# Performance work log

Hardware: AMD Instinct MI355X
Metric: run time of the kernel (lower is better)

Reference implementation:

```python
import jax, jax.numpy as jnp
import numpy as np

N = 100000      # number of nodes
D = 64          # node_dim
H = 128         # hidden
E = 1600000     # number of undirected edges (each yields 2 directed messages)


def setup_inputs() -> dict:
    key = jax.random.key(0)
    k_nodes, k_edges, k_w1, k_w2 = jax.random.split(key, 4)
    nodes = jax.random.normal(k_nodes, (N, D), dtype=jnp.float32)
    edges = jax.random.randint(k_edges, (E, 2), 0, N, dtype=jnp.int32)
    # msg = Linear(2D, H) -> ReLU -> Linear(H, D); Kaiming-ish init
    W1 = jax.random.normal(k_w1, (2 * D, H), dtype=jnp.float32) * (1.0 / np.sqrt(2 * D))
    b1 = jnp.zeros((H,), dtype=jnp.float32)
    W2 = jax.random.normal(k_w2, (H, D), dtype=jnp.float32) * (1.0 / np.sqrt(H))
    b2 = jnp.zeros((D,), dtype=jnp.float32)
    return {"nodes": nodes, "edges": edges, "W1": W1, "b1": b1, "W2": W2, "b2": b2}


def reference(nodes, edges, W1, b1, W2, b2):
    # nodes: [N, D]; edges: [E, 2] int32
    i = edges[:, 0]
    j = edges[:, 1]
    h_i = nodes[i]            # [E, D] gather
    h_j = nodes[j]            # [E, D] gather

    def mlp(x):               # [E, 2D] -> [E, D]
        return jax.nn.relu(x @ W1 + b1) @ W2 + b2

    m_ij = mlp(jnp.concatenate([h_i, h_j], axis=-1))  # message to node i
    m_ji = mlp(jnp.concatenate([h_j, h_i], axis=-1))  # message to node j

    # out = nodes.clone(); out[i] += m_ij; out[j] += m_ji  (all from ORIGINAL nodes)
    out = nodes \
        + jax.ops.segment_sum(m_ij, i, num_segments=N) \
        + jax.ops.segment_sum(m_ji, j, num_segments=N)
    return out
```

## Files before the change

### kernel.cpp

```cpp
#include <hip/hip_runtime.h>

#define NEDGES 1600000
#define NNODES 100000
#define OVCAP  (1 << 19)

typedef __bf16 bf16x8 __attribute__((ext_vector_type(8)));
typedef __bf16 bf16x4 __attribute__((ext_vector_type(4)));
typedef float f32x4 __attribute__((ext_vector_type(4)));
typedef unsigned short u16x8 __attribute__((ext_vector_type(8)));

__device__ __forceinline__ __bf16 f2bf(float f) {
  unsigned u = __builtin_bit_cast(unsigned, f);
  u += 0x7FFFu + ((u >> 16) & 1u);
  unsigned short s = (unsigned short)(u >> 16);
  return __builtin_bit_cast(__bf16, s);
}


__device__ __forceinline__ void cvt_row(const float* __restrict__ nodes, int t,
                                        __bf16* __restrict__ nbf) {
  float4 v0 = ((const float4*)nodes)[t * 2];
  float4 v1 = ((const float4*)nodes)[t * 2 + 1];
  bf16x8 o;
  o[0] = f2bf(v0.x); o[1] = f2bf(v0.y); o[2] = f2bf(v0.z); o[3] = f2bf(v0.w);
  o[4] = f2bf(v1.x); o[5] = f2bf(v1.y); o[6] = f2bf(v1.z); o[7] = f2bf(v1.w);
  ((bf16x8*)nbf)[t] = o;
}

__device__ __forceinline__ void weight_img(const float* __restrict__ W1,
                                           const float* __restrict__ W2,
                                           int t, __bf16* __restrict__ wimg) {
  if (t < 16384) {
    int k = t >> 7, n = t & 127;
    wimg[n * 128 + (((k >> 3) ^ (n & 15)) << 3) + (k & 7)] = f2bf(W1[t]);
  } else if (t < 24576) {
    int u = t - 16384;
    int k = u >> 6, n = u & 63;
    wimg[16384 + n * 128 + (((k >> 3) ^ (n & 15)) << 3) + (k & 7)] = f2bf(W2[u]);
  }
}


__global__ void zero_k(unsigned* __restrict__ cnt, unsigned* __restrict__ ovn) {
  int g = blockIdx.x * 256 + threadIdx.x;
  if (g < NNODES) cnt[g] = 0u;
  if (g == 0) *ovn = 0u;
}

__global__ void build_k(const float* __restrict__ nodes,
                        const int* __restrict__ edges,
                        const float* __restrict__ W1,
                        const float* __restrict__ W2,
                        unsigned* __restrict__ cnt,
                        unsigned* __restrict__ rec,
                        unsigned* __restrict__ ovf,
                        unsigned* __restrict__ ovn,
                        __bf16* __restrict__ wimg,
                        __bf16* __restrict__ nbf,
                        int cap) {
  const int t = blockIdx.x * 256 + threadIdx.x;
  cvt_row(nodes, t, nbf);
  weight_img(W1, W2, t, wimg);
  int4 e = ((const int4*)edges)[t];
  unsigned s0 = atomicAdd(&cnt[e.x], 1u);
  unsigned s1 = atomicAdd(&cnt[e.y], 1u);
  unsigned s2 = atomicAdd(&cnt[e.z], 1u);
  unsigned s3 = atomicAdd(&cnt[e.w], 1u);
  if ((int)s0 < cap) rec[(long)e.x * cap + s0] = (unsigned)e.y;
  else { unsigned p = atomicAdd(ovn, 1u);
         if (p < OVCAP) { ovf[2 * p] = (unsigned)e.x; ovf[2 * p + 1] = (unsigned)e.y; } }
  if ((int)s1 < cap) rec[(long)e.y * cap + s1] = (unsigned)e.x;
  else { unsigned p = atomicAdd(ovn, 1u);
         if (p < OVCAP) { ovf[2 * p] = (unsigned)e.y; ovf[2 * p + 1] = (unsigned)e.x; } }
  if ((int)s2 < cap) rec[(long)e.z * cap + s2] = (unsigned)e.w;
  else { unsigned p = atomicAdd(ovn, 1u);
         if (p < OVCAP) { ovf[2 * p] = (unsigned)e.z; ovf[2 * p + 1] = (unsigned)e.w; } }
  if ((int)s3 < cap) rec[(long)e.w * cap + s3] = (unsigned)e.z;
  else { unsigned p = atomicAdd(ovn, 1u);
         if (p < OVCAP) { ovf[2 * p] = (unsigned)e.w; ovf[2 * p + 1] = (unsigned)e.z; } }
}

__global__ void ovf_k(const float* __restrict__ nodes,
                      const float* __restrict__ W1, const float* __restrict__ b1,
                      const float* __restrict__ W2, const float* __restrict__ b2,
                      const unsigned* __restrict__ ovf,
                      const unsigned* __restrict__ ovn,
                      float* __restrict__ out) {
  unsigned n = *ovn; if (n > OVCAP) n = OVCAP;
  const unsigned total = n * 64u;
  for (unsigned idx = blockIdx.x * blockDim.x + threadIdx.x; idx < total;
       idx += gridDim.x * blockDim.x) {
    const unsigned r = idx >> 6; const int d = (int)(idx & 63u);
    const int v = (int)ovf[2 * r], u = (int)ovf[2 * r + 1];
    const float* hv = nodes + (long)v * 64;
    const float* hu = nodes + (long)u * 64;
    float md = b2[d];
    for (int h = 0; h < 128; ++h) {
      float s = b1[h];
      for (int k = 0; k < 64; ++k)
        s += hv[k] * W1[k * 128 + h] + hu[k] * W1[(64 + k) * 128 + h];
      s = s > 0.f ? s : 0.f;
      md += s * W2[h * 64 + d];
    }
    atomicAdd(out + (long)v * 64 + d, md);
  }
}

__launch_bounds__(256, 2)
__global__ void gnn_k(const __bf16* __restrict__ nbf,
                      const float* __restrict__ nodes,
                      const unsigned* __restrict__ cntoff,
                      const unsigned* __restrict__ rec,
                      const __bf16* __restrict__ wimg,
                      const float* __restrict__ b1,
                      const float* __restrict__ b2,
                      float* __restrict__ out) {
  __shared__ __align__(16) __bf16 w1t[128 * 128];
  __shared__ __align__(16) __bf16 w2t[64 * 128];
  __shared__ __align__(16) __bf16 hid[4][16 * 128];

  const int tid = threadIdx.x;

  {
    const u16x8* s1 = (const u16x8*)wimg;
    u16x8* d1 = (u16x8*)w1t;
#pragma unroll
    for (int it = 0; it < 8; ++it) d1[it * 256 + tid] = s1[it * 256 + tid];
    const u16x8* s2 = (const u16x8*)(wimg + 16384);
    u16x8* d2 = (u16x8*)w2t;
#pragma unroll
    for (int it = 0; it < 4; ++it) d2[it * 256 + tid] = s2[it * 256 + tid];
  }
  __syncthreads();

  const int lane = tid & 63, wave = tid >> 6;
  const int col = lane & 15, quad = lane >> 4;
  __bf16* myhid = hid[wave];

  const float b2l = b2[lane];

  const int bid = blockIdx.x;
  const int wg = (bid & 7) * 3125 + (bid >> 3);
  const int v = wg * 4 + wave;

  const unsigned c = cntoff[v];
  const int deg = (c < 64u) ? (int)c : 64;
  const long base = (long)v * 64;
  const int ntile = (deg + 15) >> 4;

  int ridx = v;
  if (lane < deg) ridx = (int)rec[base + lane];

  f32x4 accv[8];
  {
    const bf16x8* vrow = (const bf16x8*)(nbf + (long)v * 64);
    const bf16x8 v0f = vrow[quad];
    const bf16x8 v1f = vrow[4 + quad];
#pragma unroll
    for (int nt = 0; nt < 8; ++nt)
      accv[nt] = *(const f32x4*)&b1[nt * 16 + quad * 4];
#pragma unroll
    for (int kt = 0; kt < 2; ++kt) {
      const int kblk = kt * 4 + quad;
      const bf16x8 bx = kt ? v1f : v0f;
#pragma unroll
      for (int nt = 0; nt < 8; ++nt) {
        const int n = nt * 16 + col;
        const bf16x8 aw = *(const bf16x8*)&w1t[n * 128 + ((kblk ^ (n & 15)) << 3)];
        accv[nt] = __builtin_amdgcn_mfma_f32_16x16x32_bf16(aw, bx, accv[nt], 0, 0, 0);
      }
    }
  }

  float part[4] = {0.f, 0.f, 0.f, 0.f};

  bf16x8 a2, a3;
  {
    const int o0n = __shfl(ridx, col, 64);
    const bf16x8* orow = (const bf16x8*)(nbf + (long)o0n * 64);
    a2 = orow[quad]; a3 = orow[4 + quad];
  }

  for (int t = 0; t < ntile; ++t) {
    const int tb = t * 16;

    const int onx = __shfl(ridx, (tb + 16 + col) & 63, 64);
    const bf16x8* prow = (const bf16x8*)(nbf + (long)onx * 64);
    const bf16x8 p2 = prow[quad];
    const bf16x8 p3 = prow[4 + quad];

#pragma unroll
    for (int nt = 0; nt < 8; ++nt) {
      const int n = nt * 16 + col;
      const bf16x8 A2 = *(const bf16x8*)&w1t[n * 128 + (((8 + quad) ^ (n & 15)) << 3)];
      const bf16x8 A3 = *(const bf16x8*)&w1t[n * 128 + (((12 + quad) ^ (n & 15)) << 3)];
      f32x4 h = __builtin_amdgcn_mfma_f32_16x16x32_bf16(A2, a2, accv[nt], 0, 0, 0);
      h = __builtin_amdgcn_mfma_f32_16x16x32_bf16(A3, a3, h, 0, 0, 0);
      bf16x4 hp;
#pragma unroll
      for (int r = 0; r < 4; ++r) {
        float x = h[r];
        hp[r] = f2bf(x > 0.0f ? x : 0.0f);
      }
      const int hblk = nt * 2 + (quad >> 1);
      *(bf16x4*)&myhid[col * 128 + ((hblk ^ col) << 3) + ((quad & 1) << 2)] = hp;
    }

    f32x4 acc2[4];
#pragma unroll
    for (int nt = 0; nt < 4; ++nt) acc2[nt] = (f32x4)0.0f;
#pragma unroll
    for (int kt = 0; kt < 4; ++kt) {
      const int kblk = kt * 4 + quad;
      const bf16x8 ah = *(const bf16x8*)&myhid[col * 128 + ((kblk ^ col) << 3)];
#pragma unroll
      for (int nt = 0; nt < 4; ++nt) {
        const int n = nt * 16 + col;
        const bf16x8 bw = *(const bf16x8*)&w2t[n * 128 + ((kblk ^ (n & 15)) << 3)];
        acc2[nt] = __builtin_amdgcn_mfma_f32_16x16x32_bf16(ah, bw, acc2[nt], 0, 0, 0);
      }
    }

    if (tb + 16 <= deg) {
#pragma unroll
      for (int nt = 0; nt < 4; ++nt)
        part[nt] += (acc2[nt][0] + acc2[nt][1]) + (acc2[nt][2] + acc2[nt][3]);
    } else {
#pragma unroll
      for (int r = 0; r < 4; ++r) {
        const bool valid = (tb + quad * 4 + r) < deg;
#pragma unroll
        for (int nt = 0; nt < 4; ++nt) part[nt] += valid ? acc2[nt][r] : 0.0f;
      }
    }

    a2 = p2; a3 = p3;
  }

#pragma unroll
  for (int nt = 0; nt < 4; ++nt) {
    part[nt] += __shfl_xor(part[nt], 16, 64);
    part[nt] += __shfl_xor(part[nt], 32, 64);
  }
  const float v01 = (quad & 1) ? part[1] : part[0];
  const float v23 = (quad & 1) ? part[3] : part[2];
  const float val = (quad & 2) ? v23 : v01;

  const long o = (long)v * 64 + lane;
  out[o] = nodes[o] + val + (float)deg * b2l;
}

__launch_bounds__(256, 2)
__global__ void gnn_csr_k(const __bf16* __restrict__ nbf,
                          const float* __restrict__ nodes,
                          const unsigned* __restrict__ off,
                          const unsigned* __restrict__ rec,
                          const __bf16* __restrict__ wimg,
                          const float* __restrict__ b1,
                          const float* __restrict__ b2,
                          float* __restrict__ out) {
  __shared__ __align__(16) __bf16 w1t[128 * 128];
  __shared__ __align__(16) __bf16 w2t[64 * 128];
  __shared__ __align__(16) __bf16 hid[4][16 * 128];

  const int tid = threadIdx.x;
  {
    const u16x8* s1 = (const u16x8*)wimg;
    u16x8* d1 = (u16x8*)w1t;
#pragma unroll
    for (int it = 0; it < 8; ++it) d1[it * 256 + tid] = s1[it * 256 + tid];
    const u16x8* s2 = (const u16x8*)(wimg + 16384);
    u16x8* d2 = (u16x8*)w2t;
#pragma unroll
    for (int it = 0; it < 4; ++it) d2[it * 256 + tid] = s2[it * 256 + tid];
  }
  __syncthreads();

  const int lane = tid & 63, wave = tid >> 6;
  const int col = lane & 15, quad = lane >> 4;
  __bf16* myhid = hid[wave];
  const float b2l = b2[lane];

  const int bid = blockIdx.x;
  const int wg = (bid & 7) * 3125 + (bid >> 3);
  const int v = wg * 4 + wave;

  const unsigned o0 = off[v];
  const int deg = (int)(off[v + 1] - o0);
  const long base = (long)o0;
  const int ntile = (deg + 15) >> 4;

  f32x4 accv[8];
  {
    const bf16x8* vrow = (const bf16x8*)(nbf + (long)v * 64);
    const bf16x8 v0f = vrow[quad];
    const bf16x8 v1f = vrow[4 + quad];
#pragma unroll
    for (int nt = 0; nt < 8; ++nt)
      accv[nt] = *(const f32x4*)&b1[nt * 16 + quad * 4];
#pragma unroll
    for (int kt = 0; kt < 2; ++kt) {
      const int kblk = kt * 4 + quad;
      const bf16x8 bx = kt ? v1f : v0f;
#pragma unroll
      for (int nt = 0; nt < 8; ++nt) {
        const int n = nt * 16 + col;
        const bf16x8 aw = *(const bf16x8*)&w1t[n * 128 + ((kblk ^ (n & 15)) << 3)];
        accv[nt] = __builtin_amdgcn_mfma_f32_16x16x32_bf16(aw, bx, accv[nt], 0, 0, 0);
      }
    }
  }

  float part[4] = {0.f, 0.f, 0.f, 0.f};

  bf16x8 a2, a3;
  {
    int o0n = v;
    if (col < deg) o0n = (int)rec[base + col];
    const bf16x8* orow = (const bf16x8*)(nbf + (long)o0n * 64);
    a2 = orow[quad]; a3 = orow[4 + quad];
  }

  for (int t = 0; t < ntile; ++t) {
    const int tb = t * 16;
    int onx = v;
    {
      const int rr = tb + 16 + col;
      if (rr < deg) onx = (int)rec[base + rr];
    }
    const bf16x8* prow = (const bf16x8*)(nbf + (long)onx * 64);
    const bf16x8 p2 = prow[quad];
    const bf16x8 p3 = prow[4 + quad];

#pragma unroll
    for (int nt = 0; nt < 8; ++nt) {
      const int n = nt * 16 + col;
      const bf16x8 A2 = *(const bf16x8*)&w1t[n * 128 + (((8 + quad) ^ (n & 15)) << 3)];
      const bf16x8 A3 = *(const bf16x8*)&w1t[n * 128 + (((12 + quad) ^ (n & 15)) << 3)];
      f32x4 h = __builtin_amdgcn_mfma_f32_16x16x32_bf16(A2, a2, accv[nt], 0, 0, 0);
      h = __builtin_amdgcn_mfma_f32_16x16x32_bf16(A3, a3, h, 0, 0, 0);
      bf16x4 hp;
#pragma unroll
      for (int r = 0; r < 4; ++r) {
        float x = h[r];
        hp[r] = f2bf(x > 0.0f ? x : 0.0f);
      }
      const int hblk = nt * 2 + (quad >> 1);
      *(bf16x4*)&myhid[col * 128 + ((hblk ^ col) << 3) + ((quad & 1) << 2)] = hp;
    }

    f32x4 acc2[4];
#pragma unroll
    for (int nt = 0; nt < 4; ++nt) acc2[nt] = (f32x4)0.0f;
#pragma unroll
    for (int kt = 0; kt < 4; ++kt) {
      const int kblk = kt * 4 + quad;
      const bf16x8 ah = *(const bf16x8*)&myhid[col * 128 + ((kblk ^ col) << 3)];
#pragma unroll
      for (int nt = 0; nt < 4; ++nt) {
        const int n = nt * 16 + col;
        const bf16x8 bw = *(const bf16x8*)&w2t[n * 128 + ((kblk ^ (n & 15)) << 3)];
        acc2[nt] = __builtin_amdgcn_mfma_f32_16x16x32_bf16(ah, bw, acc2[nt], 0, 0, 0);
      }
    }

    if (tb + 16 <= deg) {
#pragma unroll
      for (int nt = 0; nt < 4; ++nt)
        part[nt] += (acc2[nt][0] + acc2[nt][1]) + (acc2[nt][2] + acc2[nt][3]);
    } else {
#pragma unroll
      for (int r = 0; r < 4; ++r) {
        const bool valid = (tb + quad * 4 + r) < deg;
#pragma unroll
        for (int nt = 0; nt < 4; ++nt) part[nt] += valid ? acc2[nt][r] : 0.0f;
      }
    }

    a2 = p2; a3 = p3;
  }

#pragma unroll
  for (int nt = 0; nt < 4; ++nt) {
    part[nt] += __shfl_xor(part[nt], 16, 64);
    part[nt] += __shfl_xor(part[nt], 32, 64);
  }
  const float v01 = (quad & 1) ? part[1] : part[0];
  const float v23 = (quad & 1) ? part[3] : part[2];
  const float val = (quad & 2) ? v23 : v01;

  const long o = (long)v * 64 + lane;
  out[o] = nodes[o] + val + (float)deg * b2l;
}


__global__ void prep_k(const float* __restrict__ nodes,
                       const float* __restrict__ W1,
                       const float* __restrict__ W2,
                       unsigned* __restrict__ cnt,
                       __bf16* __restrict__ wimg,
                       __bf16* __restrict__ nbf) {
  const int t = blockIdx.x * 256 + threadIdx.x;
  cvt_row(nodes, t, nbf);
  if (t < NNODES) cnt[t] = 0u;
  weight_img(W1, W2, t, wimg);
}

__global__ void hist_k(const int* __restrict__ edges, unsigned* __restrict__ cnt) {
  const int t = blockIdx.x * 256 + threadIdx.x;
  int4 e = ((const int4*)edges)[t];
  atomicAdd(&cnt[e.x], 1u); atomicAdd(&cnt[e.y], 1u);
  atomicAdd(&cnt[e.z], 1u); atomicAdd(&cnt[e.w], 1u);
}

__global__ void scanA_k(const unsigned* __restrict__ cnt, unsigned* __restrict__ bsum) {
  __shared__ unsigned s[1024];
  const int tid = threadIdx.x;
  const int g = blockIdx.x * 1024 + tid;
  s[tid] = (g < NNODES) ? cnt[g] : 0u;
  __syncthreads();
  for (int d = 512; d > 0; d >>= 1) {
    if (tid < d) s[tid] += s[tid + d];
    __syncthreads();
  }
  if (tid == 0) bsum[blockIdx.x] = s[0];
}

__global__ void scanB_k(const unsigned* __restrict__ cnt,
                        const unsigned* __restrict__ bsum,
                        unsigned* __restrict__ off, unsigned* __restrict__ cur) {
  __shared__ unsigned s[1024];
  const int tid = threadIdx.x;
  const int b = blockIdx.x;
  const int g = b * 1024 + tid;
  unsigned pfx = 0;
  for (int j = 0; j < b; ++j) pfx += bsum[j];
  const unsigned x = (g < NNODES) ? cnt[g] : 0u;
  s[tid] = x;
  __syncthreads();
  for (int d = 1; d < 1024; d <<= 1) {
    unsigned tv = (tid >= d) ? s[tid - d] : 0u;
    __syncthreads();
    s[tid] += tv;
    __syncthreads();
  }
  const unsigned excl = pfx + s[tid] - x;
  if (g < NNODES) { off[g] = excl; cur[g] = excl; }
  if (g == NNODES - 1) off[NNODES] = excl + x;
}

__global__ void scat_k(const int* __restrict__ edges,
                       unsigned* __restrict__ cur, unsigned* __restrict__ rec) {
  const int t = blockIdx.x * 256 + threadIdx.x;
  int4 e = ((const int4*)edges)[t];
#pragma unroll
  for (int h = 0; h < 2; ++h) {
    const int a = h ? e.z : e.x;
    const int b = h ? e.w : e.y;
    rec[atomicAdd(&cur[a], 1u)] = (unsigned)b;
    rec[atomicAdd(&cur[b], 1u)] = (unsigned)a;
  }
}


__global__ void init_out(const float* __restrict__ nodes, float* __restrict__ out) {
  int i = blockIdx.x * blockDim.x + threadIdx.x;
  ((float4*)out)[i] = ((const float4*)nodes)[i];
}

__launch_bounds__(256, 2)
__global__ void edge_mlp(const float* __restrict__ nodes,
                         const int* __restrict__ edges,
                         const float* __restrict__ W1,
                         const float* __restrict__ b1,
                         const float* __restrict__ W2,
                         const float* __restrict__ b2,
                         float* __restrict__ out) {
  __shared__ __bf16 w1t[128 * 128];
  __shared__ __bf16 w2t[64 * 128];
  __shared__ __bf16 hid[4][16 * 128];

  const int tid = threadIdx.x;

  for (int it = 0; it < 16; ++it) {
    int q = it * 256 + tid;
    int k = q >> 5;
    int nc = (q & 31) << 2;
    float4 v = ((const float4*)W1)[q];
    float vv[4] = {v.x, v.y, v.z, v.w};
#pragma unroll
    for (int c = 0; c < 4; ++c) {
      int n = nc + c;
      int blk = (k >> 3) ^ (n & 15);
      w1t[n * 128 + blk * 8 + (k & 7)] = f2bf(vv[c]);
    }
  }
  for (int it = 0; it < 8; ++it) {
    int q = it * 256 + tid;
    int k = q >> 4;
    int nc = (q & 15) << 2;
    float4 v = ((const float4*)W2)[q];
    float vv[4] = {v.x, v.y, v.z, v.w};
#pragma unroll
    for (int c = 0; c < 4; ++c) {
      int n = nc + c;
      int blk = (k >> 3) ^ (n & 15);
      w2t[n * 128 + blk * 8 + (k & 7)] = f2bf(vv[c]);
    }
  }
  __syncthreads();

  const int lane = tid & 63;
  const int wave = tid >> 6;
  const int col = lane & 15;
  const int quad = lane >> 4;
  __bf16* myhid = hid[wave];

  float b1v[8], b2v[4];
#pragma unroll
  for (int nt = 0; nt < 8; ++nt) b1v[nt] = b1[nt * 16 + col];
#pragma unroll
  for (int nt = 0; nt < 4; ++nt) b2v[nt] = b2[nt * 16 + col];

  for (int t = 0; t < 8; ++t) {
    const int e0 = blockIdx.x * 512 + wave * 128 + t * 16;
    const int e = e0 + col;
    const int ie = edges[2 * e];
    const int je = edges[2 * e + 1];

    bf16x8 af[4];
#pragma unroll
    for (int kt = 0; kt < 4; ++kt) {
      int k = kt * 32 + quad * 8;
      const float* src = (k < 64) ? (nodes + (long)ie * 64 + k)
                                  : (nodes + (long)je * 64 + (k - 64));
      float4 v0 = ((const float4*)src)[0];
      float4 v1 = ((const float4*)src)[1];
      bf16x8 a;
      a[0] = f2bf(v0.x); a[1] = f2bf(v0.y); a[2] = f2bf(v0.z); a[3] = f2bf(v0.w);
      a[4] = f2bf(v1.x); a[5] = f2bf(v1.y); a[6] = f2bf(v1.z); a[7] = f2bf(v1.w);
      af[kt] = a;
    }

#pragma unroll
    for (int dir = 0; dir < 2; ++dir) {
      f32x4 acc[8];
#pragma unroll
      for (int nt = 0; nt < 8; ++nt) acc[nt] = (f32x4)0.0f;
#pragma unroll
      for (int kt = 0; kt < 4; ++kt) {
        int kblk = kt * 4 + quad;
        if (dir) kblk ^= 8;
#pragma unroll
        for (int nt = 0; nt < 8; ++nt) {
          int n = nt * 16 + col;
          const bf16x8 bf = *(const bf16x8*)&w1t[n * 128 + ((kblk ^ (n & 15)) << 3)];
          acc[nt] = __builtin_amdgcn_mfma_f32_16x16x32_bf16(af[kt], bf, acc[nt], 0, 0, 0);
        }
      }
#pragma unroll
      for (int nt = 0; nt < 8; ++nt) {
        int unit = nt * 16 + col;
#pragma unroll
        for (int r = 0; r < 4; ++r) {
          int m = quad * 4 + r;
          float h = acc[nt][r] + b1v[nt];
          h = h > 0.0f ? h : 0.0f;
          myhid[m * 128 + (((unit >> 3) ^ m) << 3) + (unit & 7)] = f2bf(h);
        }
      }

      f32x4 acc2[4];
#pragma unroll
      for (int nt = 0; nt < 4; ++nt) acc2[nt] = (f32x4)0.0f;
#pragma unroll
      for (int kt = 0; kt < 4; ++kt) {
        int kblk = kt * 4 + quad;
        const bf16x8 ah = *(const bf16x8*)&myhid[col * 128 + ((kblk ^ col) << 3)];
#pragma unroll
        for (int nt = 0; nt < 4; ++nt) {
          int n = nt * 16 + col;
          const bf16x8 bf = *(const bf16x8*)&w2t[n * 128 + ((kblk ^ (n & 15)) << 3)];
          acc2[nt] = __builtin_amdgcn_mfma_f32_16x16x32_bf16(ah, bf, acc2[nt], 0, 0, 0);
        }
      }

#pragma unroll
      for (int r = 0; r < 4; ++r) {
        int em = quad * 4 + r;
        int node = __shfl(dir == 0 ? ie : je, em, 64);
        float* dst = out + (long)node * 64;
#pragma unroll
        for (int nt = 0; nt < 4; ++nt) {
          atomicAdd(dst + nt * 16 + col, acc2[nt][r] + b2v[nt]);
        }
      }
    }
  }
}


extern "C" void kernel_launch(void* const* d_in, const int* in_sizes, int n_in,
                              void* d_out, int out_size, void* d_ws, size_t ws_size,
                              hipStream_t stream) {
  const float* nodes = (const float*)d_in[0];
  const int*   edges = (const int*)d_in[1];
  const float* W1    = (const float*)d_in[2];
  const float* b1    = (const float*)d_in[3];
  const float* W2    = (const float*)d_in[4];
  const float* b2    = (const float*)d_in[5];
  float* out = (float*)d_out;

  char* w = (char*)d_ws;
  auto al = [](size_t x) { return (x + 255) & ~(size_t)255; };

  const int CAP = 64;

  size_t o = 0;
  unsigned* cnt = (unsigned*)(w + o); o = al(o + (size_t)NNODES * 4);
  unsigned* ovn = (unsigned*)(w + o); o = al(o + 256);
  __bf16* wimg  = (__bf16*)(w + o);   o = al(o + (size_t)24576 * 2);
  __bf16* nbf   = (__bf16*)(w + o);   o = al(o + (size_t)NNODES * 64 * 2);
  unsigned* ovf = (unsigned*)(w + o); o = al(o + (size_t)OVCAP * 2 * 4);
  unsigned* rec2 = (unsigned*)(w + o);
  const size_t need_bucket = o + (size_t)NNODES * CAP * 4;

  size_t c = (size_t)((char*)ovf - w);
  unsigned* off  = (unsigned*)(w + c); c = al(c + ((size_t)NNODES + 1) * 4);
  unsigned* cur  = (unsigned*)(w + c); c = al(c + (size_t)NNODES * 4);
  unsigned* bsum = (unsigned*)(w + c); c = al(c + 128 * 4);
  unsigned* rec  = (unsigned*)(w + c);
  const size_t need_csr = c + (size_t)2 * NEDGES * 4;

  if (d_ws && ws_size >= need_bucket) {
    zero_k<<<391, 256, 0, stream>>>(cnt, ovn);
    build_k<<<3125, 256, 0, stream>>>(nodes, edges, W1, W2, cnt, rec2, ovf, ovn,
                                      wimg, nbf, CAP);
    gnn_k<<<25000, 256, 0, stream>>>(nbf, nodes, cnt, rec2, wimg, b1, b2, out);
    ovf_k<<<104, 256, 0, stream>>>(nodes, W1, b1, W2, b2, ovf, ovn, out);
  } else if (d_ws && ws_size >= need_csr) {
    prep_k<<<3125, 256, 0, stream>>>(nodes, W1, W2, cnt, wimg, nbf);
    hist_k<<<1563, 256, 0, stream>>>(edges, cnt);
    scanA_k<<<98, 1024, 0, stream>>>(cnt, bsum);
    scanB_k<<<98, 1024, 0, stream>>>(cnt, bsum, off, cur);
    scat_k<<<1563, 256, 0, stream>>>(edges, cur, rec);
    gnn_csr_k<<<25000, 256, 0, stream>>>(nbf, nodes, off, rec, wimg, b1, b2, out);
  } else {
    init_out<<<6250, 256, 0, stream>>>(nodes, out);
    edge_mlp<<<3125, 256, 0, stream>>>(nodes, edges, W1, b1, W2, b2, out);
  }
}
```

Before: 639.0 us.

## Replicate adjacency bucket counters across eight sub-tables to cut atomic contention

Builds the per-node neighbour buckets in eight replicas selected by block index, each with a 16-slot capacity, so atomic counter increments for the same node spread over different addresses. The gather kernel reads all eight sub-counts, compacts the valid neighbour indices with ballot and popcount into LDS scratch, and sends anything past 64 neighbours to the overflow path. The CSR fallback is removed and zeroing is folded into a prep kernel. Exchanges contention for a larger workspace (8x counters, 8x16 slots per node), an extra prep launch, and more scattered index reads in the gather kernel.

```diff
diff --git a/kernel.cpp b/kernel.cpp
--- a/kernel.cpp
+++ b/kernel.cpp
@@ -3,6 +3,8 @@
 #define NEDGES 1600000
 #define NNODES 100000
 #define OVCAP  (1 << 19)
+#define NREP   8
+#define CAPSUB 16
 
 typedef __bf16 bf16x8 __attribute__((ext_vector_type(8)));
 typedef __bf16 bf16x4 __attribute__((ext_vector_type(4)));
@@ -38,6 +40,257 @@
     int k = u >> 6, n = u & 63;
     wimg[16384 + n * 128 + (((k >> 3) ^ (n & 15)) << 3) + (k & 7)] = f2bf(W2[u]);
   }
+}
+
+
+__global__ void prep8_k(const float* __restrict__ nodes,
+                        const float* __restrict__ W1,
+                        const float* __restrict__ W2,
+                        unsigned* __restrict__ cntr,
+                        unsigned* __restrict__ ovn,
+                        __bf16* __restrict__ wimg,
+                        __bf16* __restrict__ nbf) {
+  const int t = blockIdx.x * 256 + threadIdx.x;
+  cvt_row(nodes, t, nbf);
+  weight_img(W1, W2, t, wimg);
+  cntr[t] = 0u;
+  if (t == 0) *ovn = 0u;
+}
+
+__global__ void build8_k(const float* __restrict__ nodes,
+                         const int* __restrict__ edges,
+                         const float* __restrict__ W1,
+                         const float* __restrict__ W2,
+                         unsigned* __restrict__ cntr,
+                         unsigned* __restrict__ recr,
+                         unsigned* __restrict__ ovf,
+                         unsigned* __restrict__ ovn,
+                         __bf16* __restrict__ wimg,
+                         __bf16* __restrict__ nbf) {
+  const int t = blockIdx.x * 256 + threadIdx.x;
+  cvt_row(nodes, t, nbf);
+  weight_img(W1, W2, t, wimg);
+  const long cb = (long)(blockIdx.x & 7) * NNODES;
+  int4 e = ((const int4*)edges)[t];
+  unsigned s0 = atomicAdd(&cntr[cb + e.x], 1u);
+  unsigned s1 = atomicAdd(&cntr[cb + e.y], 1u);
+  unsigned s2 = atomicAdd(&cntr[cb + e.z], 1u);
+  unsigned s3 = atomicAdd(&cntr[cb + e.w], 1u);
+  if (s0 < CAPSUB) recr[(cb + e.x) * CAPSUB + s0] = (unsigned)e.y;
+  else { unsigned q = atomicAdd(ovn, 1u);
+         if (q < OVCAP) { ovf[2 * q] = (unsigned)e.x; ovf[2 * q + 1] = (unsigned)e.y; } }
+  if (s1 < CAPSUB) recr[(cb + e.y) * CAPSUB + s1] = (unsigned)e.x;
+  else { unsigned q = atomicAdd(ovn, 1u);
+         if (q < OVCAP) { ovf[2 * q] = (unsigned)e.y; ovf[2 * q + 1] = (unsigned)e.x; } }
+  if (s2 < CAPSUB) recr[(cb + e.z) * CAPSUB + s2] = (unsigned)e.w;
+  else { unsigned q = atomicAdd(ovn, 1u);
+         if (q < OVCAP) { ovf[2 * q] = (unsigned)e.z; ovf[2 * q + 1] = (unsigned)e.w; } }
+  if (s3 < CAPSUB) recr[(cb + e.w) * CAPSUB + s3] = (unsigned)e.z;
+  else { unsigned q = atomicAdd(ovn, 1u);
+         if (q < OVCAP) { ovf[2 * q] = (unsigned)e.w; ovf[2 * q + 1] = (unsigned)e.z; } }
+}
+
+__global__ void ovf_k(const float* __restrict__ nodes,
+                      const float* __restrict__ W1, const float* __restrict__ b1,
+                      const float* __restrict__ W2, const float* __restrict__ b2,
+                      const unsigned* __restrict__ ovf,
+                      const unsigned* __restrict__ ovn,
+                      float* __restrict__ out) {
+  unsigned n = *ovn; if (n > OVCAP) n = OVCAP;
+  const unsigned total = n * 64u;
+  for (unsigned idx = blockIdx.x * blockDim.x + threadIdx.x; idx < total;
+       idx += gridDim.x * blockDim.x) {
+    const unsigned r = idx >> 6; const int d = (int)(idx & 63u);
+    const int v = (int)ovf[2 * r], u = (int)ovf[2 * r + 1];
+    const float* hv = nodes + (long)v * 64;
+    const float* hu = nodes + (long)u * 64;
+    float md = b2[d];
+    for (int h = 0; h < 128; ++h) {
+      float s = b1[h];
+      for (int k = 0; k < 64; ++k)
+        s += hv[k] * W1[k * 128 + h] + hu[k] * W1[(64 + k) * 128 + h];
+      s = s > 0.f ? s : 0.f;
+      md += s * W2[h * 64 + d];
+    }
+    atomicAdd(out + (long)v * 64 + d, md);
+  }
+}
+
+__launch_bounds__(256, 2)
+__global__ void gnn8_k(const __bf16* __restrict__ nbf,
+                       const float* __restrict__ nodes,
+                       const unsigned* __restrict__ cntr,
+                       const unsigned* __restrict__ recr,
+                       const __bf16* __restrict__ wimg,
+                       const float* __restrict__ b1,
+                       const float* __restrict__ b2,
+                       unsigned* __restrict__ ovf,
+                       unsigned* __restrict__ ovn,
+                       float* __restrict__ out) {
+  __shared__ __align__(16) __bf16 w1t[128 * 128];
+  __shared__ __align__(16) __bf16 w2t[64 * 128];
+  __shared__ __align__(16) __bf16 hid[4][16 * 128];
+
+  const int tid = threadIdx.x;
+
+  {
+    const u16x8* s1 = (const u16x8*)wimg;
+    u16x8* d1 = (u16x8*)w1t;
+#pragma unroll
+    for (int it = 0; it < 8; ++it) d1[it * 256 + tid] = s1[it * 256 + tid];
+    const u16x8* s2 = (const u16x8*)(wimg + 16384);
+    u16x8* d2 = (u16x8*)w2t;
+#pragma unroll
+    for (int it = 0; it < 4; ++it) d2[it * 256 + tid] = s2[it * 256 + tid];
+  }
+  __syncthreads();
+
+  const int lane = tid & 63, wave = tid >> 6;
+  const int col = lane & 15, quad = lane >> 4;
+  __bf16* myhid = hid[wave];
+
+  const float b2l = b2[lane];
+
+  const int bid = blockIdx.x;
+  const int wg = (bid & 7) * 3125 + (bid >> 3);
+  const int v = wg * 4 + wave;
+
+  unsigned cr = 0u;
+  if (lane < NREP) cr = cntr[(long)lane * NNODES + v];
+
+  const int s0 = lane >> 4, sl = lane & 15;
+  unsigned c0 = (unsigned)__shfl((int)cr, s0, 64);
+  unsigned c1 = (unsigned)__shfl((int)cr, s0 + 4, 64);
+  if (c0 > CAPSUB) c0 = CAPSUB;
+  if (c1 > CAPSUB) c1 = CAPSUB;
+  const bool val0 = (unsigned)sl < c0;
+  const bool val1 = (unsigned)sl < c1;
+  unsigned i0 = 0u, i1 = 0u;
+  if (val0) i0 = recr[((long)s0 * NNODES + v) * CAPSUB + sl];
+  if (val1) i1 = recr[((long)(s0 + 4) * NNODES + v) * CAPSUB + sl];
+  const unsigned long long m0 = __ballot(val0);
+  const unsigned long long m1 = __ballot(val1);
+  const unsigned long long lt = (1ull << lane) - 1ull;
+  const int nb0 = __popcll(m0);
+  const int degall = nb0 + __popcll(m1);
+  const int deg = degall < 64 ? degall : 64;
+  unsigned* scratch = (unsigned*)myhid;
+  {
+    const int p0 = __popcll(m0 & lt);
+    if (val0) {
+      if (p0 < 64) scratch[p0] = i0;
+      else { unsigned q = atomicAdd(ovn, 1u);
+             if (q < OVCAP) { ovf[2 * q] = (unsigned)v; ovf[2 * q + 1] = i0; } }
+    }
+    const int p1 = nb0 + __popcll(m1 & lt);
+    if (val1) {
+      if (p1 < 64) scratch[p1] = i1;
+      else { unsigned q = atomicAdd(ovn, 1u);
+             if (q < OVCAP) { ovf[2 * q] = (unsigned)v; ovf[2 * q + 1] = i1; } }
+    }
+  }
+  int ridx = v;
+  if (lane < deg) ridx = (int)scratch[lane];
+
+  const int ntile = (deg + 15) >> 4;
+
+  f32x4 accv[8];
+  {
+    const bf16x8* vrow = (const bf16x8*)(nbf + (long)v * 64);
+    const bf16x8 v0f = vrow[quad];
+    const bf16x8 v1f = vrow[4 + quad];
+#pragma unroll
+    for (int nt = 0; nt < 8; ++nt)
+      accv[nt] = *(const f32x4*)&b1[nt * 16 + quad * 4];
+#pragma unroll
+    for (int kt = 0; kt < 2; ++kt) {
+      const int kblk = kt * 4 + quad;
+      const bf16x8 bx = kt ? v1f : v0f;
+#pragma unroll
+      for (int nt = 0; nt < 8; ++nt) {
+        const int n = nt * 16 + col;
+        const bf16x8 aw = *(const bf16x8*)&w1t[n * 128 + ((kblk ^ (n & 15)) << 3)];
+        accv[nt] = __builtin_amdgcn_mfma_f32_16x16x32_bf16(aw, bx, accv[nt], 0, 0, 0);
+      }
+    }
+  }
+
+  float part[4] = {0.f, 0.f, 0.f, 0.f};
+
+  bf16x8 a2, a3;
+  {
+    const int o0n = __shfl(ridx, col, 64);
+    const bf16x8* orow = (const bf16x8*)(nbf + (long)o0n * 64);
+    a2 = orow[quad]; a3 = orow[4 + quad];
+  }
+
+  for (int t = 0; t < ntile; ++t) {
+    const int tb = t * 16;
+
+    const int onx = __shfl(ridx, (tb + 16 + col) & 63, 64);
+    const bf16x8* prow = (const bf16x8*)(nbf + (long)onx * 64);
+    const bf16x8 p2 = prow[quad];
+    const bf16x8 p3 = prow[4 + quad];
+
+#pragma unroll
+    for (int nt = 0; nt < 8; ++nt) {
+      const int n = nt * 16 + col;
+      const bf16x8 A2 = *(const bf16x8*)&w1t[n * 128 + (((8 + quad) ^ (n & 15)) << 3)];
+      const bf16x8 A3 = *(const bf16x8*)&w1t[n * 128 + (((12 + quad) ^ (n & 15)) << 3)];
+      f32x4 h = __builtin_amdgcn_mfma_f32_16x16x32_bf16(A2, a2, accv[nt], 0, 0, 0);
+      h = __builtin_amdgcn_mfma_f32_16x16x32_bf16(A3, a3, h, 0, 0, 0);
+      bf16x4 hp;
+#pragma unroll
+      for (int r = 0; r < 4; ++r) {
+        float x = h[r];
+        hp[r] = f2bf(x > 0.0f ? x : 0.0f);
+      }
+      const int hblk = nt * 2 + (quad >> 1);
+      *(bf16x4*)&myhid[col * 128 + ((hblk ^ col) << 3) + ((quad & 1) << 2)] = hp;
+    }
+
+    f32x4 acc2[4];
+#pragma unroll
+    for (int nt = 0; nt < 4; ++nt) acc2[nt] = (f32x4)0.0f;
+#pragma unroll
+    for (int kt = 0; kt < 4; ++kt) {
+      const int kblk = kt * 4 + quad;
+      const bf16x8 ah = *(const bf16x8*)&myhid[col * 128 + ((kblk ^ col) << 3)];
+#pragma unroll
+      for (int nt = 0; nt < 4; ++nt) {
+        const int n = nt * 16 + col;
+        const bf16x8 bw = *(const bf16x8*)&w2t[n * 128 + ((kblk ^ (n & 15)) << 3)];
+        acc2[nt] = __builtin_amdgcn_mfma_f32_16x16x32_bf16(ah, bw, acc2[nt], 0, 0, 0);
+      }
+    }
+
+    if (tb + 16 <= deg) {
+#pragma unroll
+      for (int nt = 0; nt < 4; ++nt)
+        part[nt] += (acc2[nt][0] + acc2[nt][1]) + (acc2[nt][2] + acc2[nt][3]);
+    } else {
+#pragma unroll
+      for (int r = 0; r < 4; ++r) {
+        const bool valid = (tb + quad * 4 + r) < deg;
+#pragma unroll
+        for (int nt = 0; nt < 4; ++nt) part[nt] += valid ? acc2[nt][r] : 0.0f;
+      }
+    }
+
+    a2 = p2; a3 = p3;
+  }
+
+#pragma unroll
+  for (int nt = 0; nt < 4; ++nt) {
+    part[nt] += __shfl_xor(part[nt], 16, 64);
+    part[nt] += __shfl_xor(part[nt], 32, 64);
+  }
+  const float v01 = (quad & 1) ? part[1] : part[0];
+  const float v23 = (quad & 1) ? part[3] : part[2];
+  const float val = (quad & 2) ? v23 : v01;
+
+  const long o = (long)v * 64 + lane;
+  out[o] = nodes[o] + val + (float)deg * b2l;
 }
 
 
@@ -80,32 +333,6 @@
          if (p < OVCAP) { ovf[2 * p] = (unsigned)e.w; ovf[2 * p + 1] = (unsigned)e.z; } }
 }
 
-__global__ void ovf_k(const float* __restrict__ nodes,
-                      const float* __restrict__ W1, const float* __restrict__ b1,
-                      const float* __restrict__ W2, const float* __restrict__ b2,
-                      const unsigned* __restrict__ ovf,
-                      const unsigned* __restrict__ ovn,
-                      float* __restrict__ out) {
-  unsigned n = *ovn; if (n > OVCAP) n = OVCAP;
-  const unsigned total = n * 64u;
-  for (unsigned idx = blockIdx.x * blockDim.x + threadIdx.x; idx < total;
-       idx += gridDim.x * blockDim.x) {
-    const unsigned r = idx >> 6; const int d = (int)(idx & 63u);
-    const int v = (int)ovf[2 * r], u = (int)ovf[2 * r + 1];
-    const float* hv = nodes + (long)v * 64;
-    const float* hu = nodes + (long)u * 64;
-    float md = b2[d];
-    for (int h = 0; h < 128; ++h) {
-      float s = b1[h];
-      for (int k = 0; k < 64; ++k)
-        s += hv[k] * W1[k * 128 + h] + hu[k] * W1[(64 + k) * 128 + h];
-      s = s > 0.f ? s : 0.f;
-      md += s * W2[h * 64 + d];
-    }
-    atomicAdd(out + (long)v * 64 + d, md);
-  }
-}
-
 __launch_bounds__(256, 2)
 __global__ void gnn_k(const __bf16* __restrict__ nbf,
                       const float* __restrict__ nodes,
@@ -120,7 +347,6 @@
   __shared__ __align__(16) __bf16 hid[4][16 * 128];
 
   const int tid = threadIdx.x;
-
   {
     const u16x8* s1 = (const u16x8*)wimg;
     u16x8* d1 = (u16x8*)w1t;
@@ -136,7 +362,6 @@
   const int lane = tid & 63, wave = tid >> 6;
   const int col = lane & 15, quad = lane >> 4;
   __bf16* myhid = hid[wave];
-
   const float b2l = b2[lane];
 
   const int bid = blockIdx.x;
@@ -183,7 +408,6 @@
 
   for (int t = 0; t < ntile; ++t) {
     const int tb = t * 16;
-
     const int onx = __shfl(ridx, (tb + 16 + col) & 63, 64);
     const bf16x8* prow = (const bf16x8*)(nbf + (long)onx * 64);
     const bf16x8 p2 = prow[quad];
@@ -248,218 +472,6 @@
 
   const long o = (long)v * 64 + lane;
   out[o] = nodes[o] + val + (float)deg * b2l;
-}
-
-__launch_bounds__(256, 2)
-__global__ void gnn_csr_k(const __bf16* __restrict__ nbf,
-                          const float* __restrict__ nodes,
-                          const unsigned* __restrict__ off,
-                          const unsigned* __restrict__ rec,
-                          const __bf16* __restrict__ wimg,
-                          const float* __restrict__ b1,
-                          const float* __restrict__ b2,
-                          float* __restrict__ out) {
-  __shared__ __align__(16) __bf16 w1t[128 * 128];
-  __shared__ __align__(16) __bf16 w2t[64 * 128];
-  __shared__ __align__(16) __bf16 hid[4][16 * 128];
-
-  const int tid = threadIdx.x;
-  {
-    const u16x8* s1 = (const u16x8*)wimg;
-    u16x8* d1 = (u16x8*)w1t;
-#pragma unroll
-    for (int it = 0; it < 8; ++it) d1[it * 256 + tid] = s1[it * 256 + tid];
-    const u16x8* s2 = (const u16x8*)(wimg + 16384);
-    u16x8* d2 = (u16x8*)w2t;
-#pragma unroll
-    for (int it = 0; it < 4; ++it) d2[it * 256 + tid] = s2[it * 256 + tid];
-  }
-  __syncthreads();
-
-  const int lane = tid & 63, wave = tid >> 6;
-  const int col = lane & 15, quad = lane >> 4;
-  __bf16* myhid = hid[wave];
-  const float b2l = b2[lane];
-
-  const int bid = blockIdx.x;
-  const int wg = (bid & 7) * 3125 + (bid >> 3);
-  const int v = wg * 4 + wave;
-
-  const unsigned o0 = off[v];
-  const int deg = (int)(off[v + 1] - o0);
-  const long base = (long)o0;
-  const int ntile = (deg + 15) >> 4;
-
-  f32x4 accv[8];
-  {
-    const bf16x8* vrow = (const bf16x8*)(nbf + (long)v * 64);
-    const bf16x8 v0f = vrow[quad];
-    const bf16x8 v1f = vrow[4 + quad];
-#pragma unroll
-    for (int nt = 0; nt < 8; ++nt)
-      accv[nt] = *(const f32x4*)&b1[nt * 16 + quad * 4];
-#pragma unroll
-    for (int kt = 0; kt < 2; ++kt) {
-      const int kblk = kt * 4 + quad;
-      const bf16x8 bx = kt ? v1f : v0f;
-#pragma unroll
-      for (int nt = 0; nt < 8; ++nt) {
-        const int n = nt * 16 + col;
-        const bf16x8 aw = *(const bf16x8*)&w1t[n * 128 + ((kblk ^ (n & 15)) << 3)];
-        accv[nt] = __builtin_amdgcn_mfma_f32_16x16x32_bf16(aw, bx, accv[nt], 0, 0, 0);
-      }
-    }
-  }
-
-  float part[4] = {0.f, 0.f, 0.f, 0.f};
-
-  bf16x8 a2, a3;
-  {
-    int o0n = v;
-    if (col < deg) o0n = (int)rec[base + col];
-    const bf16x8* orow = (const bf16x8*)(nbf + (long)o0n * 64);
-    a2 = orow[quad]; a3 = orow[4 + quad];
-  }
-
-  for (int t = 0; t < ntile; ++t) {
-    const int tb = t * 16;
-    int onx = v;
-    {
-      const int rr = tb + 16 + col;
-      if (rr < deg) onx = (int)rec[base + rr];
-    }
-    const bf16x8* prow = (const bf16x8*)(nbf + (long)onx * 64);
-    const bf16x8 p2 = prow[quad];
-    const bf16x8 p3 = prow[4 + quad];
-
-#pragma unroll
-    for (int nt = 0; nt < 8; ++nt) {
-      const int n = nt * 16 + col;
-      const bf16x8 A2 = *(const bf16x8*)&w1t[n * 128 + (((8 + quad) ^ (n & 15)) << 3)];
-      const bf16x8 A3 = *(const bf16x8*)&w1t[n * 128 + (((12 + quad) ^ (n & 15)) << 3)];
-      f32x4 h = __builtin_amdgcn_mfma_f32_16x16x32_bf16(A2, a2, accv[nt], 0, 0, 0);
-      h = __builtin_amdgcn_mfma_f32_16x16x32_bf16(A3, a3, h, 0, 0, 0);
-      bf16x4 hp;
-#pragma unroll
-      for (int r = 0; r < 4; ++r) {
-        float x = h[r];
-        hp[r] = f2bf(x > 0.0f ? x : 0.0f);
-      }
-      const int hblk = nt * 2 + (quad >> 1);
-      *(bf16x4*)&myhid[col * 128 + ((hblk ^ col) << 3) + ((quad & 1) << 2)] = hp;
-    }
-
-    f32x4 acc2[4];
-#pragma unroll
-    for (int nt = 0; nt < 4; ++nt) acc2[nt] = (f32x4)0.0f;
-#pragma unroll
-    for (int kt = 0; kt < 4; ++kt) {
-      const int kblk = kt * 4 + quad;
-      const bf16x8 ah = *(const bf16x8*)&myhid[col * 128 + ((kblk ^ col) << 3)];
-#pragma unroll
-      for (int nt = 0; nt < 4; ++nt) {
-        const int n = nt * 16 + col;
-        const bf16x8 bw = *(const bf16x8*)&w2t[n * 128 + ((kblk ^ (n & 15)) << 3)];
-        acc2[nt] = __builtin_amdgcn_mfma_f32_16x16x32_bf16(ah, bw, acc2[nt], 0, 0, 0);
-      }
-    }
-
-    if (tb + 16 <= deg) {
-#pragma unroll
-      for (int nt = 0; nt < 4; ++nt)
-        part[nt] += (acc2[nt][0] + acc2[nt][1]) + (acc2[nt][2] + acc2[nt][3]);
-    } else {
-#pragma unroll
-      for (int r = 0; r < 4; ++r) {
-        const bool valid = (tb + quad * 4 + r) < deg;
-#pragma unroll
-        for (int nt = 0; nt < 4; ++nt) part[nt] += valid ? acc2[nt][r] : 0.0f;
-      }
-    }
-
-    a2 = p2; a3 = p3;
-  }
-
-#pragma unroll
-  for (int nt = 0; nt < 4; ++nt) {
-    part[nt] += __shfl_xor(part[nt], 16, 64);
-    part[nt] += __shfl_xor(part[nt], 32, 64);
-  }
-  const float v01 = (quad & 1) ? part[1] : part[0];
-  const float v23 = (quad & 1) ? part[3] : part[2];
-  const float val = (quad & 2) ? v23 : v01;
-
-  const long o = (long)v * 64 + lane;
-  out[o] = nodes[o] + val + (float)deg * b2l;
-}
-
-
-__global__ void prep_k(const float* __restrict__ nodes,
-                       const float* __restrict__ W1,
-                       const float* __restrict__ W2,
-                       unsigned* __restrict__ cnt,
-                       __bf16* __restrict__ wimg,
-                       __bf16* __restrict__ nbf) {
-  const int t = blockIdx.x * 256 + threadIdx.x;
-  cvt_row(nodes, t, nbf);
-  if (t < NNODES) cnt[t] = 0u;
-  weight_img(W1, W2, t, wimg);
-}
-
-__global__ void hist_k(const int* __restrict__ edges, unsigned* __restrict__ cnt) {
-  const int t = blockIdx.x * 256 + threadIdx.x;
-  int4 e = ((const int4*)edges)[t];
-  atomicAdd(&cnt[e.x], 1u); atomicAdd(&cnt[e.y], 1u);
-  atomicAdd(&cnt[e.z], 1u); atomicAdd(&cnt[e.w], 1u);
-}
-
-__global__ void scanA_k(const unsigned* __restrict__ cnt, unsigned* __restrict__ bsum) {
-  __shared__ unsigned s[1024];
-  const int tid = threadIdx.x;
-  const int g = blockIdx.x * 1024 + tid;
-  s[tid] = (g < NNODES) ? cnt[g] : 0u;
-  __syncthreads();
-  for (int d = 512; d > 0; d >>= 1) {
-    if (tid < d) s[tid] += s[tid + d];
-    __syncthreads();
-  }
-  if (tid == 0) bsum[blockIdx.x] = s[0];
-}
-
-__global__ void scanB_k(const unsigned* __restrict__ cnt,
-                        const unsigned* __restrict__ bsum,
-                        unsigned* __restrict__ off, unsigned* __restrict__ cur) {
-  __shared__ unsigned s[1024];
-  const int tid = threadIdx.x;
-  const int b = blockIdx.x;
-  const int g = b * 1024 + tid;
-  unsigned pfx = 0;
-  for (int j = 0; j < b; ++j) pfx += bsum[j];
-  const unsigned x = (g < NNODES) ? cnt[g] : 0u;
-  s[tid] = x;
-  __syncthreads();
-  for (int d = 1; d < 1024; d <<= 1) {
-    unsigned tv = (tid >= d) ? s[tid - d] : 0u;
-    __syncthreads();
-    s[tid] += tv;
-    __syncthreads();
-  }
-  const unsigned excl = pfx + s[tid] - x;
-  if (g < NNODES) { off[g] = excl; cur[g] = excl; }
-  if (g == NNODES - 1) off[NNODES] = excl + x;
-}
-
-__global__ void scat_k(const int* __restrict__ edges,
-                       unsigned* __restrict__ cur, unsigned* __restrict__ rec) {
-  const int t = blockIdx.x * 256 + threadIdx.x;
-  int4 e = ((const int4*)edges)[t];
-#pragma unroll
-  for (int h = 0; h < 2; ++h) {
-    const int a = h ? e.z : e.x;
-    const int b = h ? e.w : e.y;
-    rec[atomicAdd(&cur[a], 1u)] = (unsigned)b;
-    rec[atomicAdd(&cur[b], 1u)] = (unsigned)a;
-  }
 }
 
 
@@ -617,34 +629,36 @@
   const int CAP = 64;
 
   size_t o = 0;
-  unsigned* cnt = (unsigned*)(w + o); o = al(o + (size_t)NNODES * 4);
-  unsigned* ovn = (unsigned*)(w + o); o = al(o + 256);
-  __bf16* wimg  = (__bf16*)(w + o);   o = al(o + (size_t)24576 * 2);
-  __bf16* nbf   = (__bf16*)(w + o);   o = al(o + (size_t)NNODES * 64 * 2);
-  unsigned* ovf = (unsigned*)(w + o); o = al(o + (size_t)OVCAP * 2 * 4);
-  unsigned* rec2 = (unsigned*)(w + o);
-  const size_t need_bucket = o + (size_t)NNODES * CAP * 4;
-
-  size_t c = (size_t)((char*)ovf - w);
-  unsigned* off  = (unsigned*)(w + c); c = al(c + ((size_t)NNODES + 1) * 4);
-  unsigned* cur  = (unsigned*)(w + c); c = al(c + (size_t)NNODES * 4);
-  unsigned* bsum = (unsigned*)(w + c); c = al(c + 128 * 4);
-  unsigned* rec  = (unsigned*)(w + c);
-  const size_t need_csr = c + (size_t)2 * NEDGES * 4;
-
-  if (d_ws && ws_size >= need_bucket) {
-    zero_k<<<391, 256, 0, stream>>>(cnt, ovn);
-    build_k<<<3125, 256, 0, stream>>>(nodes, edges, W1, W2, cnt, rec2, ovf, ovn,
-                                      wimg, nbf, CAP);
-    gnn_k<<<25000, 256, 0, stream>>>(nbf, nodes, cnt, rec2, wimg, b1, b2, out);
+  unsigned* cntr = (unsigned*)(w + o); o = al(o + (size_t)NREP * NNODES * 4);
+  unsigned* ovn  = (unsigned*)(w + o); o = al(o + 256);
+  __bf16* wimg   = (__bf16*)(w + o);   o = al(o + (size_t)24576 * 2);
+  __bf16* nbf    = (__bf16*)(w + o);   o = al(o + (size_t)NNODES * 64 * 2);
+  unsigned* ovf  = (unsigned*)(w + o); o = al(o + (size_t)OVCAP * 2 * 4);
+  unsigned* recr = (unsigned*)(w + o);
+  const size_t need_rep = o + (size_t)NREP * NNODES * CAPSUB * 4;
+
+  size_t d = 0;
+  unsigned* cnt  = (unsigned*)(w + d); d = al(d + (size_t)NNODES * 4);
+  unsigned* ovn2 = (unsigned*)(w + d); d = al(d + 256);
+  __bf16* wimg2  = (__bf16*)(w + d);   d = al(d + (size_t)24576 * 2);
+  __bf16* nbf2   = (__bf16*)(w + d);   d = al(d + (size_t)NNODES * 64 * 2);
+  unsigned* ovf2 = (unsigned*)(w + d); d = al(d + (size_t)OVCAP * 2 * 4);
+  unsigned* rec2 = (unsigned*)(w + d);
+  const size_t need_bucket = d + (size_t)NNODES * CAP * 4;
+
+  if (d_ws && ws_size >= need_rep) {
+    prep8_k<<<3125, 256, 0, stream>>>(nodes, W1, W2, cntr, ovn, wimg, nbf);
+    build8_k<<<3125, 256, 0, stream>>>(nodes, edges, W1, W2, cntr, recr,
+                                       ovf, ovn, wimg, nbf);
+    gnn8_k<<<25000, 256, 0, stream>>>(nbf, nodes, cntr, recr, wimg, b1, b2,
+                                      ovf, ovn, out);
     ovf_k<<<104, 256, 0, stream>>>(nodes, W1, b1, W2, b2, ovf, ovn, out);
-  } else if (d_ws && ws_size >= need_csr) {
-    prep_k<<<3125, 256, 0, stream>>>(nodes, W1, W2, cnt, wimg, nbf);
-    hist_k<<<1563, 256, 0, stream>>>(edges, cnt);
-    scanA_k<<<98, 1024, 0, stream>>>(cnt, bsum);
-    scanB_k<<<98, 1024, 0, stream>>>(cnt, bsum, off, cur);
-    scat_k<<<1563, 256, 0, stream>>>(edges, cur, rec);
-    gnn_csr_k<<<25000, 256, 0, stream>>>(nbf, nodes, off, rec, wimg, b1, b2, out);
+  } else if (d_ws && ws_size >= need_bucket) {
+    zero_k<<<391, 256, 0, stream>>>(cnt, ovn2);
+    build_k<<<3125, 256, 0, stream>>>(nodes, edges, W1, W2, cnt, rec2, ovf2,
+                                      ovn2, wimg2, nbf2, CAP);
+    gnn_k<<<25000, 256, 0, stream>>>(nbf2, nodes, cnt, rec2, wimg2, b1, b2, out);
+    ovf_k<<<104, 256, 0, stream>>>(nodes, W1, b1, W2, b2, ovf2, ovn2, out);
   } else {
     init_out<<<6250, 256, 0, stream>>>(nodes, out);
     edge_mlp<<<3125, 256, 0, stream>>>(nodes, edges, W1, b1, W2, b2, out);
```

Result: slower. 871.3 us (+36.4%).
